# Kernel optimization log

Measured on AMD Instinct MI355X. Metric: run time of the kernel, lower is better.

Reference implementation:

```python
import jax, jax.numpy as jnp
import numpy as np

H_TOK = 57
W_TOK = 57
OUT_HW = 800
NUM_MASKS = 64  # static upper bound on sam mask ids per image


def setup_inputs() -> dict:
    key = jax.random.key(0)
    k = jax.random.split(key, 6)
    B, C, C8, L = 2, 768, 96, 21
    return {
        "embeddings": jax.random.normal(k[0], (B, H_TOK * W_TOK, C), dtype=jnp.float32),
        "sam_masks_label": jax.random.randint(k[1], (B, OUT_HW, OUT_HW), 0, NUM_MASKS, dtype=jnp.int32),
        "conv1_w": jax.random.normal(k[2], (C8, C), dtype=jnp.float32) * 0.02,
        "conv1_b": jax.random.normal(k[3], (C8,), dtype=jnp.float32) * 0.02,
        "conv2_w": jax.random.normal(k[4], (L, C8), dtype=jnp.float32) * 0.02,
        "conv2_b": jax.random.normal(k[5], (L,), dtype=jnp.float32) * 0.02,
    }


def _segment_mean_add(xb, lb):
    # xb: [H, W, C8] features; lb: [H, W] int mask ids.
    C8 = xb.shape[-1]
    seg = lb.reshape(-1)                      # [HW]
    xf = xb.reshape(-1, C8)                   # [HW, C8]
    sums = jax.ops.segment_sum(xf, seg, num_segments=NUM_MASKS)          # [M, C8]
    cnt = jax.ops.segment_sum(jnp.ones_like(seg, dtype=xf.dtype), seg, num_segments=NUM_MASKS)  # [M]
    means = sums / jnp.maximum(cnt, 1.0)[:, None]                        # empty segments -> 0, skipped
    return (xf + means[seg]).reshape(xb.shape)


def reference(embeddings, sam_masks_label, conv1_w, conv1_b, conv2_w, conv2_b):
    C = conv1_w.shape[1]
    e = embeddings.reshape(-1, H_TOK, W_TOK, C)            # [B, 57, 57, C] (NHWC)
    # conv1 (1x1) + relu, channels-last
    x = jax.nn.relu(jnp.einsum("bhwc,oc->bhwo", e, conv1_w) + conv1_b)
    # bilinear resize to 800x800, align_corners=False (half-pixel) == jax 'linear'
    B, _, _, C8 = x.shape
    x = jax.image.resize(x, (B, OUT_HW, OUT_HW, C8), method="linear")
    # per-mask segment mean added back (segments are disjoint so order-free)
    x = jax.vmap(_segment_mean_add)(x, sam_masks_label)
    # conv2 (1x1), return NCHW like torch
    out = jnp.einsum("bhwc,oc->bohw", x, conv2_w) + conv2_b[None, :, None, None]
    return out
```

## Files before the change

### kernel.cpp

```cpp
#include <hip/hip_runtime.h>

#define H_TOKN 57
#define OUT_HW 800
#define NMASK 64
#define C_IN 768
#define C8N 96
#define L_OUT 21
#define NPIX 3249
#define M_TOT 6498
#define YSTR 24
#define SCALE (57.0f/800.0f)

#define BM 32
#define ESTR 40
#define HSTR 97

#define TILE_H 25
#define TILE_W 100
#define ROWS_T 4
#define COLS_T 10
#define NTAPS 40
#define YTSTR 28
#define IPAD 264
#define ZPAD 264
#define ZROWS 32
#define NSLICE 256
#define PSTR 28

#define RCSTR 28
#define MFSTR 28
#define FROWS 4

static __device__ __forceinline__ unsigned short f2bf(float f) {
  unsigned u = __float_as_uint(f);
  u += 0x7FFFu + ((u >> 16) & 1u);
  return (unsigned short)(u >> 16);
}

__global__ __launch_bounds__(256) void fused_conv_kernel(
    const float* __restrict__ e, const float* __restrict__ w1,
    const float* __restrict__ b1, const float* __restrict__ w2,
    float* __restrict__ y57)
{
  using bf16x8 = __attribute__((ext_vector_type(8))) short;
  using f32x4  = __attribute__((ext_vector_type(4))) float;
  __shared__ __align__(16) unsigned short eA[BM * ESTR];
  __shared__ __align__(16) unsigned short wB[C8N * ESTR];
  __shared__ __align__(16) float h_lds[BM * HSTR];
  __shared__ float w2_lds[L_OUT * C8N];
  __shared__ float b1_lds[C8N];

  const int tid = threadIdx.x;
  const int m0 = blockIdx.x * BM;
  const int lane = tid & 63;
  const int wv = tid >> 6;
  const int l15 = lane & 15;
  const int khi = (lane >> 4) << 3;
  const int wm = wv & 1;
  const int wn = wv >> 1;

  for (int i = tid; i < L_OUT * C8N; i += 256) w2_lds[i] = w2[i];
  if (tid < C8N) b1_lds[tid] = b1[tid];

  f32x4 acc[3];
  #pragma unroll
  for (int t = 0; t < 3; ++t) acc[t] = (f32x4){0.f, 0.f, 0.f, 0.f};

  for (int k0 = 0; k0 < C_IN; k0 += 32) {
    __syncthreads();
    {
      int r = tid >> 3, c4 = (tid & 7) << 2;
      int p = m0 + r; if (p >= M_TOT) p = M_TOT - 1;
      float4 v = *(const float4*)(e + (size_t)p * C_IN + k0 + c4);
      ushort4 s; s.x = f2bf(v.x); s.y = f2bf(v.y); s.z = f2bf(v.z); s.w = f2bf(v.w);
      *(ushort4*)&eA[r * ESTR + c4] = s;
    }
    #pragma unroll
    for (int q = 0; q < 3; ++q) {
      int f = tid + q * 256;
      int r = f >> 3, c4 = (f & 7) << 2;
      float4 v = *(const float4*)(w1 + (size_t)r * C_IN + k0 + c4);
      ushort4 s; s.x = f2bf(v.x); s.y = f2bf(v.y); s.z = f2bf(v.z); s.w = f2bf(v.w);
      *(ushort4*)&wB[r * ESTR + c4] = s;
    }
    __syncthreads();
    bf16x8 a = *(bf16x8*)&eA[(wm * 16 + l15) * ESTR + khi];
    #pragma unroll
    for (int tt = 0; tt < 3; ++tt) {
      bf16x8 b = *(bf16x8*)&wB[((wn * 3 + tt) * 16 + l15) * ESTR + khi];
      acc[tt] = __builtin_amdgcn_mfma_f32_16x16x32_bf16(a, b, acc[tt], 0, 0, 0);
    }
  }
  __syncthreads();
  #pragma unroll
  for (int tt = 0; tt < 3; ++tt) {
    int n = (wn * 3 + tt) * 16 + l15;
    float bv = b1_lds[n];
    #pragma unroll
    for (int r = 0; r < 4; ++r) {
      int pl = wm * 16 + ((lane >> 4) << 2) + r;
      h_lds[pl * HSTR + n] = fmaxf(acc[tt][r] + bv, 0.f);
    }
  }
  __syncthreads();
  for (int i = tid; i < BM * 24; i += 256) {
    int px = i & (BM - 1), l = i >> 5;
    float s = 0.f;
    if (l < L_OUT) {
      const float* hr = &h_lds[px * HSTR];
      const float* wr = &w2_lds[l * C8N];
      #pragma unroll 8
      for (int c = 0; c < C8N; ++c) s += hr[c] * wr[c];
    }
    int p = m0 + px;
    if (p < M_TOT) y57[(size_t)p * YSTR + l] = s;
  }
}

__global__ __launch_bounds__(256) void binsum_kernel(
    const int* __restrict__ labels, const float* __restrict__ y57,
    float* __restrict__ part)
{
  using bf16x8 = __attribute__((ext_vector_type(8))) short;
  using f32x4  = __attribute__((ext_vector_type(4))) float;
  __shared__ __align__(16) unsigned short It[NMASK * IPAD];
  __shared__ __align__(16) unsigned short zT[ZROWS * ZPAD];
  __shared__ __align__(16) float ytile[NTAPS * YTSTR];
  const int tid = threadIdx.x;
  const int lane = tid & 63, wv = tid >> 6;
  const int l15 = lane & 15, khi = (lane >> 4) << 3;
  const int wc0 = blockIdx.x * TILE_W;
  const int hr0 = blockIdx.y * TILE_H;
  const int b = blockIdx.z;

  for (int i = tid; i < NMASK * IPAD / 2; i += 256) ((unsigned*)It)[i] = 0u;
  for (int i = tid; i < ZROWS * ZPAD / 2; i += 256) ((unsigned*)zT)[i] = 0u;

  float thb = fminf(fmaxf((hr0 + 0.5f) * SCALE - 0.5f, 0.f), 56.f);
  const int ib = min((int)thb, 55);
  float twb = fminf(fmaxf((wc0 + 0.5f) * SCALE - 0.5f, 0.f), 56.f);
  const int jb = min((int)twb, 55);

  const float* yb = y57 + (size_t)b * NPIX * YSTR;
  for (int i = tid; i < NTAPS * 6; i += 256) {
    int t = i / 6, q = (i - t * 6) * 4;
    int r = t / COLS_T, cc = t - r * COLS_T;
    int I = min(ib + r, 56), J = min(jb + cc, 56);
    *(float4*)&ytile[t * YTSTR + q] =
        *(const float4*)(yb + ((size_t)I * H_TOKN + J) * YSTR + q);
  }

  const bool valid = tid < 250;
  const int dh = tid / 10;
  const int dwb = (tid - dh * 10) * 10;
  const int hh = hr0 + dh;
  float th = fminf(fmaxf((hh + 0.5f) * SCALE - 0.5f, 0.f), 56.f);
  int i0 = min((int)th, 55);
  const float fh = th - (float)i0;
  const int ri = i0 - ib;
  const int* lrow = labels + ((size_t)b * OUT_HW + hh) * OUT_HW;

  f32x4 acc0 = {0.f,0.f,0.f,0.f}, acc1 = {0.f,0.f,0.f,0.f};
  int prevm = 0;
  const unsigned short one = 0x3F80;

  __syncthreads();
  if (valid) zT[24 * ZPAD + tid] = one;

  for (int c = 0; c < 10; ++c) {
    if (valid) {
      int ww = wc0 + dwb + c;
      float tw = fminf(fmaxf((ww + 0.5f) * SCALE - 0.5f, 0.f), 56.f);
      int j0 = min((int)tw, 55);
      float fw = tw - (float)j0;
      int rj = j0 - jb;
      const float* t00 = &ytile[(ri * COLS_T + rj) * YTSTR];
      const float* t10 = t00 + COLS_T * YTSTR;
      float w11 = fh * fw, w10 = fh - w11, w01 = fw - w11;
      float w00 = 1.f - fh - fw + w11;
      int m = lrow[ww] & (NMASK - 1);
      #pragma unroll
      for (int q = 0; q < 6; ++q) {
        float4 A = *(const float4*)(t00 + 4 * q);
        float4 B = *(const float4*)(t00 + YTSTR + 4 * q);
        float4 C = *(const float4*)(t10 + 4 * q);
        float4 D = *(const float4*)(t10 + YTSTR + 4 * q);
        zT[(4*q+0) * ZPAD + tid] = f2bf(w00*A.x + w01*B.x + w10*C.x + w11*D.x);
        zT[(4*q+1) * ZPAD + tid] = f2bf(w00*A.y + w01*B.y + w10*C.y + w11*D.y);
        zT[(4*q+2) * ZPAD + tid] = f2bf(w00*A.z + w01*B.z + w10*C.z + w11*D.z);
        zT[(4*q+3) * ZPAD + tid] = f2bf(w00*A.w + w01*B.w + w10*C.w + w11*D.w);
      }
      It[prevm * IPAD + tid] = 0;
      It[m * IPAD + tid] = one;
      prevm = m;
    }
    __syncthreads();
    #pragma unroll
    for (int ks = 0; ks < 8; ++ks) {
      bf16x8 a  = *(bf16x8*)&It[(wv * 16 + l15) * IPAD + ks * 32 + khi];
      bf16x8 b0 = *(bf16x8*)&zT[l15 * ZPAD + ks * 32 + khi];
      bf16x8 b1 = *(bf16x8*)&zT[(16 + l15) * ZPAD + ks * 32 + khi];
      acc0 = __builtin_amdgcn_mfma_f32_16x16x32_bf16(a, b0, acc0, 0, 0, 0);
      acc1 = __builtin_amdgcn_mfma_f32_16x16x32_bf16(a, b1, acc1, 0, 0, 0);
    }
    __syncthreads();
  }

  float* pb = part + ((size_t)b * NSLICE +
                      (size_t)(blockIdx.y * gridDim.x + blockIdx.x)) * (NMASK * PSTR);
  const int g4 = (lane >> 4) << 2;
  #pragma unroll
  for (int r = 0; r < 4; ++r) {
    int m = wv * 16 + g4 + r;
    pb[m * PSTR + l15] = acc0[r];
    if (l15 <= 8) pb[m * PSTR + 16 + l15] = acc1[r];
  }
}

__global__ __launch_bounds__(256) void reduce_kernel(
    const float* __restrict__ part, const float* __restrict__ b2,
    float* __restrict__ meanFg)
{
  const int bm = blockIdx.x;
  const int b = bm >> 6, m = bm & 63;
  const int tid = threadIdx.x;
  const float* p = part + ((size_t)b * NSLICE + tid) * (NMASK * PSTR) + (size_t)m * PSTR;
  float4 v[7];
  #pragma unroll
  for (int q = 0; q < 7; ++q) v[q] = *(const float4*)(p + q * 4);
  #pragma unroll
  for (int off = 32; off > 0; off >>= 1) {
    #pragma unroll
    for (int q = 0; q < 7; ++q) {
      v[q].x += __shfl_down(v[q].x, off, 64);
      v[q].y += __shfl_down(v[q].y, off, 64);
      v[q].z += __shfl_down(v[q].z, off, 64);
      v[q].w += __shfl_down(v[q].w, off, 64);
    }
  }
  __shared__ float s_red[4][28];
  const int wid = tid >> 6, lane = tid & 63;
  if (lane == 0) {
    #pragma unroll
    for (int q = 0; q < 7; ++q) *(float4*)&s_red[wid][q * 4] = v[q];
  }
  __syncthreads();
  if (tid < 28) {
    float cnt = s_red[0][24] + s_red[1][24] + s_red[2][24] + s_red[3][24];
    float t = s_red[0][tid] + s_red[1][tid] + s_red[2][tid] + s_red[3][tid];
    float out = (tid < L_OUT) ? t / fmaxf(cnt, 1.f) + b2[tid] : 0.f;
    meanFg[(size_t)bm * MFSTR + tid] = out;
  }
}

__global__ __launch_bounds__(256) void final_kernel(
    const float* __restrict__ y57, const int* __restrict__ labels,
    const float* __restrict__ meanFg, float* __restrict__ out)
{
  __shared__ __align__(16) float rowC[FROWS][H_TOKN * RCSTR];
  __shared__ __align__(16) float meanF[NMASK * MFSTR];
  const int tid = threadIdx.x;
  const int hh0 = blockIdx.y * FROWS;
  const int b = blockIdx.z;
  const float* yb = y57 + (size_t)b * NPIX * YSTR;

  for (int i = tid; i < FROWS * H_TOKN * 6; i += 256) {
    int r = i / (H_TOKN * 6);
    int rest = i - r * (H_TOKN * 6);
    int rr = rest / 6, q = (rest - rr * 6) * 4;
    float th = fminf(fmaxf((hh0 + r + 0.5f) * SCALE - 0.5f, 0.f), 56.f);
    int i0 = min((int)th, 55);
    float fh = th - (float)i0;
    const float* s0 = yb + ((size_t)i0 * H_TOKN + rr) * YSTR + q;
    float4 A = *(const float4*)s0;
    float4 B = *(const float4*)(s0 + H_TOKN * YSTR);
    *(float4*)&rowC[r][rr * RCSTR + q] = make_float4(
        A.x + fh * (B.x - A.x), A.y + fh * (B.y - A.y),
        A.z + fh * (B.z - A.z), A.w + fh * (B.w - A.w));
  }
  {
    const float* src = meanFg + (size_t)b * NMASK * MFSTR;
    for (int i = tid; i < NMASK * MFSTR / 4; i += 256)
      *(float4*)&meanF[i * 4] = *(const float4*)(src + i * 4);
  }
  __syncthreads();

  for (int g = tid; g < FROWS * 200; g += 256) {
    const int row = g / 200;
    const int gg = g - row * 200;
    const int w0 = gg * 4;
    const int hh = hh0 + row;
    const int* lrow = labels + ((size_t)b * OUT_HW + hh) * OUT_HW;
    int4 la = *(const int4*)(lrow + w0);
    float* ob = out + (size_t)b * L_OUT * OUT_HW * OUT_HW + (size_t)hh * OUT_HW + w0;
    const float* rc = rowC[row];

    float fwv[4]; const float* c0p[4]; const float* mfp[4];
    {
      int lam[4] = {la.x & 63, la.y & 63, la.z & 63, la.w & 63};
      #pragma unroll
      for (int k = 0; k < 4; ++k) {
        float tw = fminf(fmaxf((w0 + k + 0.5f) * SCALE - 0.5f, 0.f), 56.f);
        int j0 = min((int)tw, 55);
        fwv[k] = tw - (float)j0;
        c0p[k] = &rc[j0 * RCSTR];
        mfp[k] = &meanF[lam[k] * MFSTR];
      }
    }
    #pragma unroll
    for (int q = 0; q < 6; ++q) {
      float4 V[4];
      #pragma unroll
      for (int k = 0; k < 4; ++k) {
        float4 A  = *(const float4*)(c0p[k] + 4 * q);
        float4 Bv = *(const float4*)(c0p[k] + RCSTR + 4 * q);
        float4 Mv = *(const float4*)(mfp[k] + 4 * q);
        V[k].x = A.x + fwv[k] * (Bv.x - A.x) + Mv.x;
        V[k].y = A.y + fwv[k] * (Bv.y - A.y) + Mv.y;
        V[k].z = A.z + fwv[k] * (Bv.z - A.z) + Mv.z;
        V[k].w = A.w + fwv[k] * (Bv.w - A.w) + Mv.w;
      }
      const int l = 4 * q;
      *(float4*)(ob + (size_t)l * 640000) = make_float4(V[0].x, V[1].x, V[2].x, V[3].x);
      if (l + 1 < L_OUT)
        *(float4*)(ob + (size_t)(l+1) * 640000) = make_float4(V[0].y, V[1].y, V[2].y, V[3].y);
      if (l + 2 < L_OUT)
        *(float4*)(ob + (size_t)(l+2) * 640000) = make_float4(V[0].z, V[1].z, V[2].z, V[3].z);
      if (l + 3 < L_OUT)
        *(float4*)(ob + (size_t)(l+3) * 640000) = make_float4(V[0].w, V[1].w, V[2].w, V[3].w);
    }
  }
}

extern "C" void kernel_launch(void* const* d_in, const int* in_sizes, int n_in,
                              void* d_out, int out_size, void* d_ws, size_t ws_size,
                              hipStream_t stream)
{
  const float* e   = (const float*)d_in[0];
  const int*   lab = (const int*)d_in[1];
  const float* w1  = (const float*)d_in[2];
  const float* b1  = (const float*)d_in[3];
  const float* w2  = (const float*)d_in[4];
  const float* b2  = (const float*)d_in[5];
  float* out = (float*)d_out;
  float* ws  = (float*)d_ws;

  float* y57_ws = ws;
  float* part   = y57_ws + (size_t)M_TOT * YSTR;
  float* meanFg = part + (size_t)2 * NSLICE * NMASK * PSTR;

  fused_conv_kernel<<<dim3((M_TOT + BM - 1) / BM), 256, 0, stream>>>(
      e, w1, b1, w2, y57_ws);
  binsum_kernel<<<dim3(OUT_HW / TILE_W, OUT_HW / TILE_H, 2), 256, 0, stream>>>(
      lab, y57_ws, part);
  reduce_kernel<<<dim3(2 * NMASK), 256, 0, stream>>>(part, b2, meanFg);
  final_kernel<<<dim3(1, OUT_HW / FROWS, 2), 256, 0, stream>>>(
      y57_ws, lab, meanFg, out);
}
```

Measured before the change: 71.94 us.

## Restructure final kernel per output channel with channel-planar intermediate layout

The conv kernel now also writes a channel-planar copy of the low-res projected features, and the reduce kernel writes per-channel transposed mask means. The final kernel is relaunched with one block per (channel, 16-row strip, batch). Each thread writes one float4 along a row of a single output plane, so stores are contiguous instead of scattered across 21 planes. In exchange, labels are re-read once per output channel (21 times), and the extra transposed write adds a little work to the conv kernel.

```diff
diff --git a/kernel.cpp b/kernel.cpp
--- a/kernel.cpp
+++ b/kernel.cpp
@@ -9,6 +9,7 @@
 #define NPIX 3249
 #define M_TOT 6498
 #define YSTR 24
+#define TPLANE 3264
 #define SCALE (57.0f/800.0f)
 
 #define BM 32
@@ -27,9 +28,8 @@
 #define NSLICE 256
 #define PSTR 28
 
-#define RCSTR 28
-#define MFSTR 28
-#define FROWS 4
+#define FR 16
+#define RCL 60
 
 static __device__ __forceinline__ unsigned short f2bf(float f) {
   unsigned u = __float_as_uint(f);
@@ -40,7 +40,7 @@
 __global__ __launch_bounds__(256) void fused_conv_kernel(
     const float* __restrict__ e, const float* __restrict__ w1,
     const float* __restrict__ b1, const float* __restrict__ w2,
-    float* __restrict__ y57)
+    float* __restrict__ y57, float* __restrict__ y57T)
 {
   using bf16x8 = __attribute__((ext_vector_type(8))) short;
   using f32x4  = __attribute__((ext_vector_type(4))) float;
@@ -113,7 +113,14 @@
       for (int c = 0; c < C8N; ++c) s += hr[c] * wr[c];
     }
     int p = m0 + px;
-    if (p < M_TOT) y57[(size_t)p * YSTR + l] = s;
+    if (p < M_TOT) {
+      y57[(size_t)p * YSTR + l] = s;
+      if (l < L_OUT) {
+        int bb = (p >= NPIX);
+        int pp = p - bb * NPIX;
+        y57T[((size_t)bb * 24 + l) * TPLANE + pp] = s;
+      }
+    }
   }
 }
 
@@ -219,7 +226,7 @@
 
 __global__ __launch_bounds__(256) void reduce_kernel(
     const float* __restrict__ part, const float* __restrict__ b2,
-    float* __restrict__ meanFg)
+    float* __restrict__ meanFgT)
 {
   const int bm = blockIdx.x;
   const int b = bm >> 6, m = bm & 63;
@@ -245,90 +252,72 @@
     for (int q = 0; q < 7; ++q) *(float4*)&s_red[wid][q * 4] = v[q];
   }
   __syncthreads();
-  if (tid < 28) {
+  if (tid < L_OUT) {
     float cnt = s_red[0][24] + s_red[1][24] + s_red[2][24] + s_red[3][24];
     float t = s_red[0][tid] + s_red[1][tid] + s_red[2][tid] + s_red[3][tid];
-    float out = (tid < L_OUT) ? t / fmaxf(cnt, 1.f) + b2[tid] : 0.f;
-    meanFg[(size_t)bm * MFSTR + tid] = out;
+    meanFgT[((size_t)b * L_OUT + tid) * NMASK + m] = t / fmaxf(cnt, 1.f) + b2[tid];
   }
 }
 
 __global__ __launch_bounds__(256) void final_kernel(
-    const float* __restrict__ y57, const int* __restrict__ labels,
-    const float* __restrict__ meanFg, float* __restrict__ out)
-{
-  __shared__ __align__(16) float rowC[FROWS][H_TOKN * RCSTR];
-  __shared__ __align__(16) float meanF[NMASK * MFSTR];
+    const float* __restrict__ y57T, const int* __restrict__ labels,
+    const float* __restrict__ meanFgT, float* __restrict__ out)
+{
+  __shared__ __align__(16) float rowCl[FR * RCL];
+  __shared__ __align__(16) float2 fwj[OUT_HW];
+  __shared__ float meanFl[NMASK];
   const int tid = threadIdx.x;
-  const int hh0 = blockIdx.y * FROWS;
+  const int l = blockIdx.x;
+  const int h0 = blockIdx.y * FR;
   const int b = blockIdx.z;
-  const float* yb = y57 + (size_t)b * NPIX * YSTR;
-
-  for (int i = tid; i < FROWS * H_TOKN * 6; i += 256) {
-    int r = i / (H_TOKN * 6);
-    int rest = i - r * (H_TOKN * 6);
-    int rr = rest / 6, q = (rest - rr * 6) * 4;
-    float th = fminf(fmaxf((hh0 + r + 0.5f) * SCALE - 0.5f, 0.f), 56.f);
+
+  for (int w = tid; w < OUT_HW; w += 256) {
+    float tw = fminf(fmaxf((w + 0.5f) * SCALE - 0.5f, 0.f), 56.f);
+    int j0 = min((int)tw, 55);
+    fwj[w] = make_float2(tw - (float)j0, __int_as_float(j0));
+  }
+  if (tid < NMASK) meanFl[tid] = meanFgT[((size_t)b * L_OUT + l) * NMASK + tid];
+  const float* yTl = y57T + ((size_t)b * 24 + l) * TPLANE;
+  for (int i = tid; i < FR * H_TOKN; i += 256) {
+    int r = i / H_TOKN, j = i - r * H_TOKN;
+    float th = fminf(fmaxf((h0 + r + 0.5f) * SCALE - 0.5f, 0.f), 56.f);
     int i0 = min((int)th, 55);
     float fh = th - (float)i0;
-    const float* s0 = yb + ((size_t)i0 * H_TOKN + rr) * YSTR + q;
-    float4 A = *(const float4*)s0;
-    float4 B = *(const float4*)(s0 + H_TOKN * YSTR);
-    *(float4*)&rowC[r][rr * RCSTR + q] = make_float4(
-        A.x + fh * (B.x - A.x), A.y + fh * (B.y - A.y),
-        A.z + fh * (B.z - A.z), A.w + fh * (B.w - A.w));
-  }
-  {
-    const float* src = meanFg + (size_t)b * NMASK * MFSTR;
-    for (int i = tid; i < NMASK * MFSTR / 4; i += 256)
-      *(float4*)&meanF[i * 4] = *(const float4*)(src + i * 4);
-  }
-  __syncthreads();
-
-  for (int g = tid; g < FROWS * 200; g += 256) {
-    const int row = g / 200;
-    const int gg = g - row * 200;
-    const int w0 = gg * 4;
-    const int hh = hh0 + row;
-    const int* lrow = labels + ((size_t)b * OUT_HW + hh) * OUT_HW;
-    int4 la = *(const int4*)(lrow + w0);
-    float* ob = out + (size_t)b * L_OUT * OUT_HW * OUT_HW + (size_t)hh * OUT_HW + w0;
-    const float* rc = rowC[row];
-
-    float fwv[4]; const float* c0p[4]; const float* mfp[4];
-    {
-      int lam[4] = {la.x & 63, la.y & 63, la.z & 63, la.w & 63};
-      #pragma unroll
-      for (int k = 0; k < 4; ++k) {
-        float tw = fminf(fmaxf((w0 + k + 0.5f) * SCALE - 0.5f, 0.f), 56.f);
-        int j0 = min((int)tw, 55);
-        fwv[k] = tw - (float)j0;
-        c0p[k] = &rc[j0 * RCSTR];
-        mfp[k] = &meanF[lam[k] * MFSTR];
-      }
-    }
-    #pragma unroll
-    for (int q = 0; q < 6; ++q) {
-      float4 V[4];
-      #pragma unroll
-      for (int k = 0; k < 4; ++k) {
-        float4 A  = *(const float4*)(c0p[k] + 4 * q);
-        float4 Bv = *(const float4*)(c0p[k] + RCSTR + 4 * q);
-        float4 Mv = *(const float4*)(mfp[k] + 4 * q);
-        V[k].x = A.x + fwv[k] * (Bv.x - A.x) + Mv.x;
-        V[k].y = A.y + fwv[k] * (Bv.y - A.y) + Mv.y;
-        V[k].z = A.z + fwv[k] * (Bv.z - A.z) + Mv.z;
-        V[k].w = A.w + fwv[k] * (Bv.w - A.w) + Mv.w;
-      }
-      const int l = 4 * q;
-      *(float4*)(ob + (size_t)l * 640000) = make_float4(V[0].x, V[1].x, V[2].x, V[3].x);
-      if (l + 1 < L_OUT)
-        *(float4*)(ob + (size_t)(l+1) * 640000) = make_float4(V[0].y, V[1].y, V[2].y, V[3].y);
-      if (l + 2 < L_OUT)
-        *(float4*)(ob + (size_t)(l+2) * 640000) = make_float4(V[0].z, V[1].z, V[2].z, V[3].z);
-      if (l + 3 < L_OUT)
-        *(float4*)(ob + (size_t)(l+3) * 640000) = make_float4(V[0].w, V[1].w, V[2].w, V[3].w);
-    }
+    float a = yTl[i0 * H_TOKN + j];
+    float c = yTl[(i0 + 1) * H_TOKN + j];
+    rowCl[r * RCL + j] = a + fh * (c - a);
+  }
+  __syncthreads();
+
+  float* ob = out + (((size_t)b * L_OUT + l) * OUT_HW + h0) * OUT_HW;
+  const int* lb = labels + ((size_t)b * OUT_HW + h0) * OUT_HW;
+  for (int g = tid; g < FR * 200; g += 256) {
+    int r = g / 200;
+    int c4 = (g - r * 200) * 4;
+    int4 la = *(const int4*)(lb + (size_t)r * OUT_HW + c4);
+    const float* rc = &rowCl[r * RCL];
+    float4 V;
+    {
+      float2 fj = fwj[c4 + 0];
+      const float* s = rc + __float_as_int(fj.y);
+      V.x = s[0] + fj.x * (s[1] - s[0]) + meanFl[la.x & 63];
+    }
+    {
+      float2 fj = fwj[c4 + 1];
+      const float* s = rc + __float_as_int(fj.y);
+      V.y = s[0] + fj.x * (s[1] - s[0]) + meanFl[la.y & 63];
+    }
+    {
+      float2 fj = fwj[c4 + 2];
+      const float* s = rc + __float_as_int(fj.y);
+      V.z = s[0] + fj.x * (s[1] - s[0]) + meanFl[la.z & 63];
+    }
+    {
+      float2 fj = fwj[c4 + 3];
+      const float* s = rc + __float_as_int(fj.y);
+      V.w = s[0] + fj.x * (s[1] - s[0]) + meanFl[la.w & 63];
+    }
+    *(float4*)(ob + (size_t)r * OUT_HW + c4) = V;
   }
 }
 
@@ -345,15 +334,16 @@
   float* out = (float*)d_out;
   float* ws  = (float*)d_ws;
 
-  float* y57_ws = ws;
-  float* part   = y57_ws + (size_t)M_TOT * YSTR;
-  float* meanFg = part + (size_t)2 * NSLICE * NMASK * PSTR;
+  float* y57_ws  = ws;
+  float* y57T_ws = y57_ws + (size_t)M_TOT * YSTR;
+  float* part    = y57T_ws + (size_t)2 * 24 * TPLANE;
+  float* meanFgT = part + (size_t)2 * NSLICE * NMASK * PSTR;
 
   fused_conv_kernel<<<dim3((M_TOT + BM - 1) / BM), 256, 0, stream>>>(
-      e, w1, b1, w2, y57_ws);
+      e, w1, b1, w2, y57_ws, y57T_ws);
   binsum_kernel<<<dim3(OUT_HW / TILE_W, OUT_HW / TILE_H, 2), 256, 0, stream>>>(
       lab, y57_ws, part);
-  reduce_kernel<<<dim3(2 * NMASK), 256, 0, stream>>>(part, b2, meanFg);
-  final_kernel<<<dim3(1, OUT_HW / FROWS, 2), 256, 0, stream>>>(
-      y57_ws, lab, meanFg, out);
-}
+  reduce_kernel<<<dim3(2 * NMASK), 256, 0, stream>>>(part, b2, meanFgT);
+  final_kernel<<<dim3(L_OUT, OUT_HW / FR, 2), 256, 0, stream>>>(
+      y57T_ws, lab, meanFgT, out);
+}
```

New measurement: 77.22 us. +7.3%, slower.
